# Kernel optimization log

Hardware: AMD Instinct MI355X
Metric: run time of the kernel (lower is better)

Reference implementation:

```python
import jax, jax.numpy as jnp
import numpy as np
from fractions import Fraction
from math import factorial

MUL = 64
IRREPS = [(MUL, 0, 1), (MUL, 1, -1), (MUL, 2, 1)]  # (mul, l, parity); same for in1/in2/out
N = 4096


def _f(n):
    return Fraction(factorial(round(n)), 1)


def _su2_cg(j1, m1, j2, m2, j3, m3):
    # Complex-basis SU(2) Clebsch-Gordan coefficient <j1 m1 j2 m2 | j3 m3> (Racah formula).
    if m3 != m1 + m2:
        return 0.0
    vmin = int(max(-j1 + j2 + m3, -j1 + m1, 0))
    vmax = int(min(j2 + j3 + m1, j3 - j1 + j2, j3 + m3))
    C = float((2 * j3 + 1) * Fraction(
        _f(j3 + j1 - j2) * _f(j3 - j1 + j2) * _f(j1 + j2 - j3) * _f(j3 + m3) * _f(j3 - m3),
        _f(j1 + j2 + j3 + 1) * _f(j1 - m1) * _f(j1 + m1) * _f(j2 - m2) * _f(j2 + m2))) ** 0.5
    S = Fraction(0)
    for v in range(vmin, vmax + 1):
        S += (-1) ** int(v + j2 + m2) * Fraction(
            _f(j2 + j3 + m1 - v) * _f(j1 - m1 + v),
            _f(v) * _f(j3 - j1 + j2 - v) * _f(j3 + m3 - v) * _f(v + j1 - j2 - m3))
    return C * float(S)


def _q(l):
    # Change of basis real -> complex spherical harmonics, with (-i)^l phase so CG is real.
    q = np.zeros((2 * l + 1, 2 * l + 1), dtype=complex)
    for m in range(-l, 0):
        q[l + m, l + abs(m)] = 1 / 2 ** 0.5
        q[l + m, l - abs(m)] = -1j / 2 ** 0.5
    q[l, l] = 1
    for m in range(1, l + 1):
        q[l + m, l + abs(m)] = (-1) ** m / 2 ** 0.5
        q[l + m, l - abs(m)] = 1j * (-1) ** m / 2 ** 0.5
    return (-1j) ** l * q


def _so3_cg(l1, l2, l3):
    # Real-basis SO(3) Clebsch-Gordan tensor, shape (2l1+1, 2l2+1, 2l3+1).
    C = np.zeros((2 * l1 + 1, 2 * l2 + 1, 2 * l3 + 1))
    for m1 in range(-l1, l1 + 1):
        for m2 in range(-l2, l2 + 1):
            for m3 in range(-l3, l3 + 1):
                C[l1 + m1, l2 + m2, l3 + m3] = _su2_cg(l1, m1, l2, m2, l3, m3)
    C = np.einsum('ij,kl,mn,ikm->jln', _q(l1), _q(l2), np.conj(_q(l3)), C)
    assert np.abs(C.imag).max() < 1e-6
    return np.ascontiguousarray(C.real.astype(np.float32))


def _offsets(irreps):
    offs, o = [], 0
    for mul, l, p in irreps:
        offs.append(o)
        o += mul * (2 * l + 1)
    return offs, o


OFF, DIM = _offsets(IRREPS)

# Enumerate fully-connected paths honoring parity and triangle selection rules.
PATHS = []
for io, (mo, lo, po) in enumerate(IRREPS):
    for i1, (m1, l1, p1) in enumerate(IRREPS):
        for i2, (m2, l2, p2) in enumerate(IRREPS):
            if p1 * p2 == po and abs(l1 - l2) <= lo <= l1 + l2:
                PATHS.append((i1, i2, io, _so3_cg(l1, l2, lo)))
N_PATHS = len(PATHS)  # 11 for this irrep layout


def setup_inputs() -> dict:
    key = jax.random.key(0)
    k1, k2, k3 = jax.random.split(key, 3)
    inputs1 = jax.random.normal(k1, (N, DIM), dtype=jnp.float32)
    inputs2 = jax.random.normal(k2, (N, DIM), dtype=jnp.float32)
    std = 1.0 / float(np.sqrt(MUL * MUL))  # per-path weight_std
    W = jax.random.normal(k3, (N_PATHS, MUL, MUL, MUL), dtype=jnp.float32) * std
    return {"inputs1": inputs1, "inputs2": inputs2, "W": W}


def _seg(x, i):
    mul, l, _ = IRREPS[i]
    d = 2 * l + 1
    return x[:, OFF[i]:OFF[i] + mul * d].reshape(x.shape[0], mul, d)


def reference(inputs1, inputs2, W):
    # out[z, w, k] = sum_{u,v,i,j} W_path[u,v,w] * CG[i,j,k] * x1[z,u,i] * x2[z,v,j]
    segs = [[] for _ in IRREPS]
    for p, (i1, i2, io, cg) in enumerate(PATHS):
        x1 = _seg(inputs1, i1)  # [z, u, i]
        x2 = _seg(inputs2, i2)  # [z, v, j]
        y = jnp.einsum('zui,zvj,ijk,uvw->zwk', x1, x2, jnp.asarray(cg), W[p], optimize=True)
        segs[io].append(y)
    out = jnp.concatenate(
        [sum(s).reshape(inputs1.shape[0], -1) for s in segs], axis=-1)
    # normalize=True: divide by sqrt(output dim), as in the source
    return out * (1.0 / float(np.sqrt(out.shape[-1])))
```

## Files before the change

kernel.cpp:

```cpp
#include <hip/hip_runtime.h>
#include <hip/hip_fp16.h>


typedef unsigned short u16;
typedef _Float16 f16;
typedef __attribute__((ext_vector_type(8))) _Float16 f16x8;
typedef __attribute__((ext_vector_type(4))) float f32x4;

#define NZ 4096
#define ROWE 832
#define ROW2 576

__device__ __forceinline__ u16 f2h(float x) {
    _Float16 v = (_Float16)x; u16 b; __builtin_memcpy(&b, &v, 2); return b;
}

constexpr u16 f2h_bits(float xf) {
    unsigned u = __builtin_bit_cast(unsigned, xf);
    unsigned sign = (u >> 16) & 0x8000u;
    int exp = (int)((u >> 23) & 0xffu) - 127 + 15;
    unsigned man = u & 0x7fffffu;
    if (exp >= 31) return (u16)(sign | 0x7c00u);
    if (exp <= 0) {
        if (exp < -10) return (u16)sign;
        man |= 0x800000u;
        int sh = 14 - exp;
        unsigned h = man >> sh;
        unsigned rem = man & ((1u << sh) - 1u);
        unsigned half = 1u << (sh - 1);
        if (rem > half || (rem == half && (h & 1u))) ++h;
        return (u16)(sign | h);
    }
    unsigned h = ((unsigned)exp << 10) | (man >> 13);
    unsigned rem = man & 0x1fffu;
    if (rem > 0x1000u || (rem == 0x1000u && (h & 1u))) ++h;
    return (u16)(sign | h);
}
__device__ __forceinline__ __half2 h2dup(unsigned bits16) {
    unsigned d = bits16 * 0x10001u;
    __half2 r; __builtin_memcpy(&r, &d, 4); return r;
}
__device__ __forceinline__ __half2 h2zero() {
    unsigned z = 0; __half2 r; __builtin_memcpy(&r, &z, 4); return r;
}

struct CGE { int i, j, k; float c; };
template<int P> struct CGT;
template<> struct CGT<0> { static constexpr int n=1; static constexpr CGE e[1]={{0,0,0,1.0f}}; };
template<> struct CGT<1> { static constexpr int n=3; static constexpr CGE e[3]={
    {0,0,0,0.5773502691896258f},{1,1,0,0.5773502691896258f},{2,2,0,0.5773502691896258f}}; };
template<> struct CGT<2> { static constexpr int n=5; static constexpr CGE e[5]={
    {0,0,0,0.4472135954999579f},{1,1,0,0.4472135954999579f},{2,2,0,0.4472135954999579f},
    {3,3,0,0.4472135954999579f},{4,4,0,0.4472135954999579f}}; };
template<> struct CGT<3> { static constexpr int n=3; static constexpr CGE e[3]={
    {0,0,0,1.0f},{0,1,1,1.0f},{0,2,2,1.0f}}; };
template<> struct CGT<4> { static constexpr int n=3; static constexpr CGE e[3]={
    {0,0,0,1.0f},{1,0,1,1.0f},{2,0,2,1.0f}}; };
template<> struct CGT<5> { static constexpr int n=11; static constexpr CGE e[11]={
    {0,2,0,-0.31622776601683794f},{1,1,0,0.5477225575051661f},{0,4,0,-0.5477225575051661f},{2,0,0,0.5477225575051661f},
    {0,1,1,0.5477225575051661f},{2,3,1,0.5477225575051661f},{1,2,1,0.6324555320336759f},
    {2,2,2,-0.31622776601683794f},{1,3,2,0.5477225575051661f},{0,0,2,0.5477225575051661f},{2,4,2,0.5477225575051661f}}; };
template<> struct CGT<6> { static constexpr int n=11; static constexpr CGE e[11]={
    {2,0,0,-0.31622776601683794f},{1,1,0,0.5477225575051661f},{4,0,0,-0.5477225575051661f},{0,2,0,0.5477225575051661f},
    {1,0,1,0.5477225575051661f},{3,2,1,0.5477225575051661f},{2,1,1,0.6324555320336759f},
    {2,2,2,-0.31622776601683794f},{3,1,2,0.5477225575051661f},{0,0,2,0.5477225575051661f},{4,2,2,0.5477225575051661f}}; };
template<> struct CGT<7> { static constexpr int n=5; static constexpr CGE e[5]={
    {0,0,0,1.0f},{0,1,1,1.0f},{0,2,2,1.0f},{0,3,3,1.0f},{0,4,4,1.0f}}; };
template<> struct CGT<8> { static constexpr int n=11; static constexpr CGE e[11]={
    {0,2,0,0.7071067811865476f},{2,0,0,0.7071067811865476f},
    {0,1,1,0.7071067811865476f},{1,0,1,0.7071067811865476f},
    {0,0,2,-0.4082482904638630f},{1,1,2,0.8164965809277260f},{2,2,2,-0.4082482904638630f},
    {1,2,3,0.7071067811865476f},{2,1,3,0.7071067811865476f},
    {0,0,4,-0.7071067811865476f},{2,2,4,0.7071067811865476f}}; };
template<> struct CGT<9> { static constexpr int n=5; static constexpr CGE e[5]={
    {0,0,0,1.0f},{1,0,1,1.0f},{2,0,2,1.0f},{3,0,3,1.0f},{4,0,4,1.0f}}; };
template<> struct CGT<10> { static constexpr int n=25; static constexpr CGE e[25]={
    {0,2,0,-0.5345224838248488f},{2,0,0,-0.5345224838248488f},{1,3,0,0.4629100498862757f},{3,1,0,0.4629100498862757f},
    {0,3,1,0.4629100498862757f},{3,0,1,0.4629100498862757f},{1,4,1,-0.4629100498862757f},{4,1,1,-0.4629100498862757f},
    {1,2,1,0.2672612419124244f},{2,1,1,0.2672612419124244f},
    {0,0,2,-0.5345224838248488f},{1,1,2,0.2672612419124244f},{2,2,2,0.5345224838248488f},{3,3,2,0.2672612419124244f},{4,4,2,-0.5345224838248488f},
    {0,1,3,0.4629100498862757f},{1,0,3,0.4629100498862757f},{3,4,3,0.4629100498862757f},{4,3,3,0.4629100498862757f},
    {2,3,3,0.2672612419124244f},{3,2,3,0.2672612419124244f},
    {1,1,4,-0.4629100498862757f},{3,3,4,0.4629100498862757f},{2,4,4,-0.5345224838248488f},{4,2,4,-0.5345224838248488f}}; };

template<int SEG>
__device__ __forceinline__ int soff(int m) {
    if constexpr (SEG == 0) return m;
    else if constexpr (SEG == 1) return 64 + 4*m;
    else return 320 + 8*m;
}
template<int SEG>
__device__ __forceinline__ int sb2(int j) {
    if constexpr (SEG == 0) return 0;
    else if constexpr (SEG == 1) return 64 + j*64;
    else return 256 + j*64;
}
template<int L>
__device__ __forceinline__ void load_a1bits(const u16* p, u16* o) {
    if constexpr (L == 0) {
        o[0] = p[0];
    } else if constexpr (L == 1) {
        uint2 r = *reinterpret_cast<const uint2*>(p);
        o[0] = (u16)(r.x & 0xffff); o[1] = (u16)(r.x >> 16); o[2] = (u16)(r.y & 0xffff);
    } else {
        uint4 r = *reinterpret_cast<const uint4*>(p);
        o[0] = (u16)(r.x & 0xffff); o[1] = (u16)(r.x >> 16);
        o[2] = (u16)(r.y & 0xffff); o[3] = (u16)(r.y >> 16);
        o[4] = (u16)(r.z & 0xffff);
    }
}

__device__ __forceinline__ void stage_chunk(const u16* __restrict__ Wtb, int g,
                                            u16* lbuf, int tid) {
    const u16* src = Wtb + ((size_t)g << 13);
    #pragma unroll
    for (int qq = 0; qq < 4; ++qq) {
        const int off = qq*2048 + tid*8;
        __builtin_amdgcn_global_load_lds(
            (const __attribute__((address_space(1))) void*)(const void*)(src + off),
            (__attribute__((address_space(3))) void*)(void*)(lbuf + off),
            16, 0, 0);
    }
}

template<int PID, int S1, int S2, int KO>
__device__ __forceinline__ void chunk_compute(const u16* __restrict__ lbuf,
                                              const u16 (&a1b)[2][2*S1+1],
                                              const __half2 (&b2h)[2][4][2*S2+1],
                                              f32x4 (&acc)[KO][4], int lane) {
    const int kb = lane >> 4, nl = lane & 15;
    #pragma unroll
    for (int uu = 0; uu < 2; ++uu) {
        __half2 a1h[2*S1+1];
        #pragma unroll
        for (int i = 0; i < 2*S1+1; ++i) a1h[i] = h2dup(a1b[uu][i]);
        __half2 pre[CGT<PID>::n];
        #pragma unroll
        for (int t = 0; t < CGT<PID>::n; ++t) {
            const u16 cb = f2h_bits(CGT<PID>::e[t].c);
            pre[t] = __hmul2(h2dup(cb), a1h[CGT<PID>::e[t].i]);
        }
        #pragma unroll
        for (int h = 0; h < 2; ++h) {
            f16x8 bf[4];
            #pragma unroll
            for (int nf = 0; nf < 4; ++nf) {
                const int w = nf*16 + nl;
                const int slot = w*16 + ((uu*8 + h*4 + kb) ^ (w & 15));
                bf[nf] = *reinterpret_cast<const f16x8*>(lbuf + slot*8);
            }
            #pragma unroll
            for (int ko = 0; ko < KO; ++ko) {
                union { __half2 h[4]; f16x8 v; } af;
                #pragma unroll
                for (int q = 0; q < 4; ++q) {
                    __half2 s = h2zero();
                    #pragma unroll
                    for (int t = 0; t < CGT<PID>::n; ++t)
                        if (CGT<PID>::e[t].k == ko)
                            s = __hfma2(pre[t], b2h[h][q][CGT<PID>::e[t].j], s);
                    af.h[q] = s;
                }
                #pragma unroll
                for (int nf = 0; nf < 4; ++nf)
                    acc[ko][nf] = __builtin_amdgcn_mfma_f32_16x16x32_f16(af.v, bf[nf], acc[ko][nf], 0, 0, 0);
            }
        }
    }
}

template<int PID, int S1, int S2, int KO>
__device__ __forceinline__ void run_path(const u16* __restrict__ x1r, const u16* __restrict__ x2r,
                                         const u16* __restrict__ Wtb, u16* lds,
                                         f32x4 (&acc)[KO][4], int lane, int tid,
                                         int cbase, int cpp, int& q, int nq, int GB) {
    constexpr int D1 = 2*S1 + 1, D2 = 2*S2 + 1;
    const int kb = lane >> 4;
    __half2 b2h[2][4][D2];
    #pragma unroll
    for (int h = 0; h < 2; ++h)
        #pragma unroll
        for (int j = 0; j < D2; ++j) {
            const u16* p = x2r + sb2<S2>(j) + h*32 + kb*8;
            uint4 r = *reinterpret_cast<const uint4*>(p);
            __builtin_memcpy(&b2h[h][0][j], &r.x, 4);
            __builtin_memcpy(&b2h[h][1][j], &r.y, 4);
            __builtin_memcpy(&b2h[h][2][j], &r.z, 4);
            __builtin_memcpy(&b2h[h][3][j], &r.w, 4);
        }

    const int ubase = cbase*2;
    u16 a1b[2][D1], a1nb[2][D1];
    #pragma unroll
    for (int uu = 0; uu < 2; ++uu)
        load_a1bits<S1>(x1r + soff<S1>(ubase + uu), a1b[uu]);

    for (int c = 0; c < cpp; ++c) {
        __syncthreads();
        const int cn = (c + 1 == cpp) ? 0 : c + 1;
        #pragma unroll
        for (int uu = 0; uu < 2; ++uu)
            load_a1bits<S1>(x1r + soff<S1>(ubase + cn*2 + uu), a1nb[uu]);
        if (q + 1 < nq) {
            const int qn = q + 1;
            const int g = GB + (qn/cpp)*32 + cbase + (qn % cpp);
            stage_chunk(Wtb, g, lds + ((qn & 1) << 13), tid);
        }
        chunk_compute<PID,S1,S2,KO>(lds + ((q & 1) << 13), a1b, b2h, acc, lane);
        #pragma unroll
        for (int uu = 0; uu < 2; ++uu)
            #pragma unroll
            for (int d = 0; d < D1; ++d) a1b[uu][d] = a1nb[uu][d];
        ++q;
    }
}

template<int IO, bool DIRECT>
__device__ __forceinline__ void run_unit(const u16* __restrict__ XB1, const u16* __restrict__ XB2,
                                         const u16* __restrict__ Wtb, float* __restrict__ dst,
                                         int zt, int cbase, int cpp, u16* lds) {
    constexpr int KO   = 2*IO + 1;
    constexpr int NP   = (IO == 0) ? 3 : 4;
    constexpr int GB   = (IO == 0) ? 0 : (IO == 1 ? 96 : 224);
    constexpr int OFFI = (IO == 0) ? 0 : (IO == 1 ? 64 : 256);
    constexpr int CO   = KO*64;
    const int tid = threadIdx.x;
    const int lane = tid & 63, wave = tid >> 6;
    const int zin = zt*64 + wave*16 + (lane & 15);
    const u16* x1r = XB1 + (size_t)zin*ROWE;
    const u16* x2r = XB2 + (size_t)zin*ROW2;
    f32x4 acc[KO][4];
    #pragma unroll
    for (int k = 0; k < KO; ++k)
        #pragma unroll
        for (int nf = 0; nf < 4; ++nf) acc[k][nf] = (f32x4){0.f, 0.f, 0.f, 0.f};

    int q = 0;
    const int nq = NP*cpp;
    stage_chunk(Wtb, GB + cbase, lds, tid);

    if constexpr (IO == 0) {
        run_path<0,0,0,KO>(x1r, x2r, Wtb, lds, acc, lane, tid, cbase, cpp, q, nq, GB);
        run_path<1,1,1,KO>(x1r, x2r, Wtb, lds, acc, lane, tid, cbase, cpp, q, nq, GB);
        run_path<2,2,2,KO>(x1r, x2r, Wtb, lds, acc, lane, tid, cbase, cpp, q, nq, GB);
    } else if constexpr (IO == 1) {
        run_path<3,0,1,KO>(x1r, x2r, Wtb, lds, acc, lane, tid, cbase, cpp, q, nq, GB);
        run_path<4,1,0,KO>(x1r, x2r, Wtb, lds, acc, lane, tid, cbase, cpp, q, nq, GB);
        run_path<5,1,2,KO>(x1r, x2r, Wtb, lds, acc, lane, tid, cbase, cpp, q, nq, GB);
        run_path<6,2,1,KO>(x1r, x2r, Wtb, lds, acc, lane, tid, cbase, cpp, q, nq, GB);
    } else {
        run_path<7,0,2,KO>(x1r, x2r, Wtb, lds, acc, lane, tid, cbase, cpp, q, nq, GB);
        run_path<8,1,1,KO>(x1r, x2r, Wtb, lds, acc, lane, tid, cbase, cpp, q, nq, GB);
        run_path<9,2,0,KO>(x1r, x2r, Wtb, lds, acc, lane, tid, cbase, cpp, q, nq, GB);
        run_path<10,2,2,KO>(x1r, x2r, Wtb, lds, acc, lane, tid, cbase, cpp, q, nq, GB);
    }

    float* lf = reinterpret_cast<float*>(lds);
    const int nl = lane & 15;
    const int hi = lane >> 4;
    #pragma unroll
    for (int round = 0; round < 4; ++round) {
        __syncthreads();
        if (wave == round) {
            const int zl = hi*4;
            #pragma unroll
            for (int k = 0; k < KO; ++k)
                #pragma unroll
                for (int nf = 0; nf < 4; ++nf) {
                    const int col = (nf*16 + nl)*KO + k;
                    #pragma unroll
                    for (int r = 0; r < 4; ++r)
                        lf[(zl + r)*CO + col] = acc[k][nf][r];
                }
        }
        __syncthreads();
        const int zbase = zt*64 + round*16;
        const int TOT4 = 4*CO;
        for (int i = tid; i < TOT4; i += 256) {
            const int zr = i / (CO/4), c4 = i % (CO/4);
            float4 v = *reinterpret_cast<const float4*>(&lf[zr*CO + c4*4]);
            if constexpr (DIRECT) {
                const float sc = 0.041666666666666664f;
                v.x *= sc; v.y *= sc; v.z *= sc; v.w *= sc;
            }
            *reinterpret_cast<float4*>(&dst[(size_t)(zbase + zr)*576 + OFFI + c4*4]) = v;
        }
    }
}

template<bool DEEP>
__global__ __launch_bounds__(256) void tp_main_split(const u16* __restrict__ XB1, const u16* __restrict__ XB2,
                                                     const u16* __restrict__ Wtb, float* __restrict__ Pbuf) {
    __shared__ u16 smem[2*8192];
    const int bid = blockIdx.x;
    int io, uq, zt, cbase, cpp;
    if constexpr (DEEP) {
        if (bid < 512)      { io = 2; uq = bid >> 6; zt = bid & 63; cbase = uq*4; cpp = 4; }
        else if (bid < 896) { const int b = bid - 512; io = 1; uq = b >> 6; zt = b & 63;
                              cbase = (uq < 2) ? uq*6 : 12 + (uq - 2)*5; cpp = (uq < 2) ? 6 : 5; }
        else                { const int b = bid - 896; io = 0; uq = b >> 6; zt = b & 63;
                              cbase = uq*8; cpp = 8; }
    } else {
        if (bid < 256)      { io = 2; uq = bid >> 6; zt = bid & 63; cbase = uq*8; cpp = 8; }
        else if (bid < 448) { const int b = bid - 256; io = 1; uq = b >> 6; zt = b & 63;
                              cbase = (uq == 0) ? 0 : (11 + 11*(uq - 1)); cpp = (uq == 2) ? 10 : 11; }
        else                { const int b = bid - 448; io = 0; uq = 0; zt = b & 63; cbase = 0; cpp = 32; }
    }
    float* dstP = Pbuf + (size_t)uq*NZ*576;
    if (io == 0)      run_unit<0,false>(XB1, XB2, Wtb, dstP, zt, cbase, cpp, smem);
    else if (io == 1) run_unit<1,false>(XB1, XB2, Wtb, dstP, zt, cbase, cpp, smem);
    else              run_unit<2,false>(XB1, XB2, Wtb, dstP, zt, cbase, cpp, smem);
}

__global__ __launch_bounds__(256) void tp_main_direct(const u16* __restrict__ XB1, const u16* __restrict__ XB2,
                                                      const u16* __restrict__ Wtb, float* __restrict__ out) {
    __shared__ u16 smem[2*8192];
    const int bid = blockIdx.x;
    const int io = 2 - (bid >> 6), zt = bid & 63;
    if (io == 0)      run_unit<0,true>(XB1, XB2, Wtb, out, zt, 0, 32, smem);
    else if (io == 1) run_unit<1,true>(XB1, XB2, Wtb, out, zt, 0, 32, smem);
    else              run_unit<2,true>(XB1, XB2, Wtb, out, zt, 0, 32, smem);
}

template<int CA, int CB, int CC>
__global__ __launch_bounds__(256) void reduce_k(const float* __restrict__ P, float* __restrict__ out) {
    const int i = blockIdx.x*256 + threadIdx.x;
    const int col0 = (i*4) % 576;
    const int cnt = (col0 < 64) ? CA : (col0 < 256 ? CB : CC);
    float4 s = reinterpret_cast<const float4*>(P)[i];
    for (int u = 1; u < cnt; ++u) {
        float4 t = reinterpret_cast<const float4*>(P + (size_t)u*NZ*576)[i];
        s.x += t.x; s.y += t.y; s.z += t.z; s.w += t.w;
    }
    const float sc = 0.041666666666666664f;
    float4 o; o.x = s.x*sc; o.y = s.y*sc; o.z = s.z*sc; o.w = s.w*sc;
    reinterpret_cast<float4*>(out)[i] = o;
}

__global__ void prep_x(const float* __restrict__ x1, const float* __restrict__ x2,
                       u16* __restrict__ XB1, u16* __restrict__ XB2) {
    int g = blockIdx.x * 256 + threadIdx.x;
    const int P1 = NZ * 192;
    const int P2 = NZ * 144;
    if (g < P1) {
        const int zz = g / 192, s = g - zz*192, seg = s >> 6, m = s & 63;
        const float* sp = x1 + (size_t)zz*576;
        u16* dp = XB1 + (size_t)zz*ROWE;
        if (seg == 0) {
            dp[m] = f2h(sp[m]);
        } else if (seg == 1) {
            u16 t0 = f2h(sp[64 + m*3 + 0]);
            u16 t1 = f2h(sp[64 + m*3 + 1]);
            u16 t2 = f2h(sp[64 + m*3 + 2]);
            uint2 pk; pk.x = (unsigned)t0 | ((unsigned)t1 << 16); pk.y = (unsigned)t2;
            *reinterpret_cast<uint2*>(dp + 64 + m*4) = pk;
        } else {
            u16 t[5];
            #pragma unroll
            for (int c = 0; c < 5; ++c) t[c] = f2h(sp[256 + m*5 + c]);
            uint4 pk;
            pk.x = (unsigned)t[0] | ((unsigned)t[1] << 16);
            pk.y = (unsigned)t[2] | ((unsigned)t[3] << 16);
            pk.z = (unsigned)t[4];
            pk.w = 0u;
            *reinterpret_cast<uint4*>(dp + 320 + m*8) = pk;
        }
    } else if (g < P1 + P2) {
        const int gg = g - P1;
        const int zz = gg / 144, c4 = gg - zz*144;
        const int col = c4*4;
        const float* sp = x2 + (size_t)zz*576;
        u16 t[4];
        #pragma unroll
        for (int qd = 0; qd < 4; ++qd) {
            const int cc = col + qd;
            int si;
            if (cc < 64)       si = cc;
            else if (cc < 256) { const int j = (cc - 64) >> 6, v = (cc - 64) & 63;  si = 64  + v*3 + j; }
            else               { const int j = (cc - 256) >> 6, v = (cc - 256) & 63; si = 256 + v*5 + j; }
            t[qd] = f2h(sp[si]);
        }
        uint2 pk;
        pk.x = (unsigned)t[0] | ((unsigned)t[1] << 16);
        pk.y = (unsigned)t[2] | ((unsigned)t[3] << 16);
        *reinterpret_cast<uint2*>(XB2 + (size_t)zz*ROW2 + col) = pk;
    }
}

__global__ void prep_w(const float* __restrict__ W, u16* __restrict__ Wtb) {
    __shared__ float ld[4096];
    const int b = blockIdx.x;
    const int p = b >> 6, u = b & 63;
    const int tid = threadIdx.x;
    const float* src = W + ((size_t)(p*64 + u) << 12);
    #pragma unroll
    for (int i = 0; i < 16; ++i) ld[tid + i*256] = src[tid + i*256];
    __syncthreads();
    const int g  = p*32 + (u >> 1);
    const int mb = (u & 1)*8;
    #pragma unroll
    for (int r = 0; r < 2; ++r) {
        const int j = r*256 + tid;
        const int w = j & 63, ms = j >> 6;
        const int m = mb + ms;
        const int h = ms >> 2, kb = ms & 3;
        const int vb = h*32 + kb*8;
        u16 tmp[8];
        #pragma unroll
        for (int e = 0; e < 8; ++e) tmp[e] = f2h(ld[(vb + e)*64 + w]);
        const int unit = w*16 + (m ^ (w & 15));
        uint4 pk;
        pk.x = (unsigned)tmp[0] | ((unsigned)tmp[1] << 16);
        pk.y = (unsigned)tmp[2] | ((unsigned)tmp[3] << 16);
        pk.z = (unsigned)tmp[4] | ((unsigned)tmp[5] << 16);
        pk.w = (unsigned)tmp[6] | ((unsigned)tmp[7] << 16);
        *reinterpret_cast<uint4*>(Wtb + (size_t)g*8192 + (size_t)unit*8) = pk;
    }
}

extern "C" void kernel_launch(void* const* d_in, const int* in_sizes, int n_in,
                              void* d_out, int out_size, void* d_ws, size_t ws_size,
                              hipStream_t stream) {
    const float* x1 = (const float*)d_in[0];
    const float* x2 = (const float*)d_in[1];
    const float* W  = (const float*)d_in[2];
    float* out = (float*)d_out;

    u16* XB1 = (u16*)d_ws;
    u16* XB2 = XB1 + (size_t)NZ*ROWE;
    u16* Wtb = XB2 + (size_t)NZ*ROW2;
    const size_t baseu = (size_t)NZ*ROWE + (size_t)NZ*ROW2 + (size_t)11*32*8192;
    if (ws_size < baseu*2) return;
    float* Pbuf = (float*)(XB1 + baseu);
    const size_t avail = ws_size - baseu*2;
    const size_t psz = (size_t)NZ*576*4;
    const bool deep     = (avail >= 8*psz);
    const bool balanced = (avail >= 4*psz);

    hipLaunchKernelGGL(prep_x, dim3((NZ*(192+144))/256), dim3(256), 0, stream, x1, x2, XB1, XB2);
    hipLaunchKernelGGL(prep_w, dim3(11*64), dim3(256), 0, stream, W, Wtb);

    if (deep) {
        hipLaunchKernelGGL(tp_main_split<true>, dim3(1152), dim3(256), 0, stream, XB1, XB2, Wtb, Pbuf);
        hipLaunchKernelGGL((reduce_k<4,6,8>), dim3(NZ*576/4/256), dim3(256), 0, stream, Pbuf, out);
    } else if (balanced) {
        hipLaunchKernelGGL(tp_main_split<false>, dim3(512), dim3(256), 0, stream, XB1, XB2, Wtb, Pbuf);
        hipLaunchKernelGGL((reduce_k<1,3,4>), dim3(NZ*576/4/256), dim3(256), 0, stream, Pbuf, out);
    } else {
        hipLaunchKernelGGL(tp_main_direct, dim3(192), dim3(256), 0, stream, XB1, XB2, Wtb, out);
    }
}
```

Baseline: 118.6 us.

## Halve weight chunk granularity and rebalance split-K work across fewer blocks

Each staged weight chunk now covers one u row (4096 halves) instead of two, with the prep_w layout, swizzle, chunk indexing and LDS buffers reworked to match, which shrinks the shared-memory footprint. The deep 1152-block split is removed. The balanced path now launches 576 blocks with 2/3/4 partial slices per output irrep, so the reduction reads fewer partials. The aim is higher occupancy from less LDS and less partial-sum traffic. The cost is twice as many barriers and chunk stages per unit of work, plus fewer blocks to hide latency.

```diff
diff --git a/kernel.cpp b/kernel.cpp
--- a/kernel.cpp
+++ b/kernel.cpp
@@ -112,9 +112,9 @@
 
 __device__ __forceinline__ void stage_chunk(const u16* __restrict__ Wtb, int g,
                                             u16* lbuf, int tid) {
-    const u16* src = Wtb + ((size_t)g << 13);
-    #pragma unroll
-    for (int qq = 0; qq < 4; ++qq) {
+    const u16* src = Wtb + ((size_t)g << 12);
+    #pragma unroll
+    for (int qq = 0; qq < 2; ++qq) {
         const int off = qq*2048 + tid*8;
         __builtin_amdgcn_global_load_lds(
             (const __attribute__((address_space(1))) void*)(const void*)(src + off),
@@ -125,46 +125,43 @@
 
 template<int PID, int S1, int S2, int KO>
 __device__ __forceinline__ void chunk_compute(const u16* __restrict__ lbuf,
-                                              const u16 (&a1b)[2][2*S1+1],
+                                              const u16 (&a1b)[2*S1+1],
                                               const __half2 (&b2h)[2][4][2*S2+1],
                                               f32x4 (&acc)[KO][4], int lane) {
     const int kb = lane >> 4, nl = lane & 15;
-    #pragma unroll
-    for (int uu = 0; uu < 2; ++uu) {
-        __half2 a1h[2*S1+1];
-        #pragma unroll
-        for (int i = 0; i < 2*S1+1; ++i) a1h[i] = h2dup(a1b[uu][i]);
-        __half2 pre[CGT<PID>::n];
-        #pragma unroll
-        for (int t = 0; t < CGT<PID>::n; ++t) {
-            const u16 cb = f2h_bits(CGT<PID>::e[t].c);
-            pre[t] = __hmul2(h2dup(cb), a1h[CGT<PID>::e[t].i]);
-        }
-        #pragma unroll
-        for (int h = 0; h < 2; ++h) {
-            f16x8 bf[4];
+    __half2 a1h[2*S1+1];
+    #pragma unroll
+    for (int i = 0; i < 2*S1+1; ++i) a1h[i] = h2dup(a1b[i]);
+    __half2 pre[CGT<PID>::n];
+    #pragma unroll
+    for (int t = 0; t < CGT<PID>::n; ++t) {
+        const u16 cb = f2h_bits(CGT<PID>::e[t].c);
+        pre[t] = __hmul2(h2dup(cb), a1h[CGT<PID>::e[t].i]);
+    }
+    #pragma unroll
+    for (int h = 0; h < 2; ++h) {
+        f16x8 bf[4];
+        #pragma unroll
+        for (int nf = 0; nf < 4; ++nf) {
+            const int w = nf*16 + nl;
+            const int slot = w*8 + ((h*4 + kb) ^ (w & 7));
+            bf[nf] = *reinterpret_cast<const f16x8*>(lbuf + slot*8);
+        }
+        #pragma unroll
+        for (int ko = 0; ko < KO; ++ko) {
+            union { __half2 h[4]; f16x8 v; } af;
             #pragma unroll
-            for (int nf = 0; nf < 4; ++nf) {
-                const int w = nf*16 + nl;
-                const int slot = w*16 + ((uu*8 + h*4 + kb) ^ (w & 15));
-                bf[nf] = *reinterpret_cast<const f16x8*>(lbuf + slot*8);
+            for (int q = 0; q < 4; ++q) {
+                __half2 s = h2zero();
+                #pragma unroll
+                for (int t = 0; t < CGT<PID>::n; ++t)
+                    if (CGT<PID>::e[t].k == ko)
+                        s = __hfma2(pre[t], b2h[h][q][CGT<PID>::e[t].j], s);
+                af.h[q] = s;
             }
             #pragma unroll
-            for (int ko = 0; ko < KO; ++ko) {
-                union { __half2 h[4]; f16x8 v; } af;
-                #pragma unroll
-                for (int q = 0; q < 4; ++q) {
-                    __half2 s = h2zero();
-                    #pragma unroll
-                    for (int t = 0; t < CGT<PID>::n; ++t)
-                        if (CGT<PID>::e[t].k == ko)
-                            s = __hfma2(pre[t], b2h[h][q][CGT<PID>::e[t].j], s);
-                    af.h[q] = s;
-                }
-                #pragma unroll
-                for (int nf = 0; nf < 4; ++nf)
-                    acc[ko][nf] = __builtin_amdgcn_mfma_f32_16x16x32_f16(af.v, bf[nf], acc[ko][nf], 0, 0, 0);
-            }
+            for (int nf = 0; nf < 4; ++nf)
+                acc[ko][nf] = __builtin_amdgcn_mfma_f32_16x16x32_f16(af.v, bf[nf], acc[ko][nf], 0, 0, 0);
         }
     }
 }
@@ -189,28 +186,21 @@
             __builtin_memcpy(&b2h[h][3][j], &r.w, 4);
         }
 
-    const int ubase = cbase*2;
-    u16 a1b[2][D1], a1nb[2][D1];
-    #pragma unroll
-    for (int uu = 0; uu < 2; ++uu)
-        load_a1bits<S1>(x1r + soff<S1>(ubase + uu), a1b[uu]);
+    u16 a1b[D1], a1nb[D1];
+    load_a1bits<S1>(x1r + soff<S1>(cbase), a1b);
 
     for (int c = 0; c < cpp; ++c) {
         __syncthreads();
         const int cn = (c + 1 == cpp) ? 0 : c + 1;
-        #pragma unroll
-        for (int uu = 0; uu < 2; ++uu)
-            load_a1bits<S1>(x1r + soff<S1>(ubase + cn*2 + uu), a1nb[uu]);
+        load_a1bits<S1>(x1r + soff<S1>(cbase + cn), a1nb);
         if (q + 1 < nq) {
             const int qn = q + 1;
-            const int g = GB + (qn/cpp)*32 + cbase + (qn % cpp);
-            stage_chunk(Wtb, g, lds + ((qn & 1) << 13), tid);
-        }
-        chunk_compute<PID,S1,S2,KO>(lds + ((q & 1) << 13), a1b, b2h, acc, lane);
-        #pragma unroll
-        for (int uu = 0; uu < 2; ++uu)
-            #pragma unroll
-            for (int d = 0; d < D1; ++d) a1b[uu][d] = a1nb[uu][d];
+            const int g = GB + (qn/cpp)*64 + cbase + (qn % cpp);
+            stage_chunk(Wtb, g, lds + ((qn & 1) << 12), tid);
+        }
+        chunk_compute<PID,S1,S2,KO>(lds + ((q & 1) << 12), a1b, b2h, acc, lane);
+        #pragma unroll
+        for (int d = 0; d < D1; ++d) a1b[d] = a1nb[d];
         ++q;
     }
 }
@@ -221,7 +211,7 @@
                                          int zt, int cbase, int cpp, u16* lds) {
     constexpr int KO   = 2*IO + 1;
     constexpr int NP   = (IO == 0) ? 3 : 4;
-    constexpr int GB   = (IO == 0) ? 0 : (IO == 1 ? 96 : 224);
+    constexpr int GB   = (IO == 0) ? 0 : (IO == 1 ? 192 : 448);
     constexpr int OFFI = (IO == 0) ? 0 : (IO == 1 ? 64 : 256);
     constexpr int CO   = KO*64;
     const int tid = threadIdx.x;
@@ -288,24 +278,16 @@
     }
 }
 
-template<bool DEEP>
 __global__ __launch_bounds__(256) void tp_main_split(const u16* __restrict__ XB1, const u16* __restrict__ XB2,
                                                      const u16* __restrict__ Wtb, float* __restrict__ Pbuf) {
-    __shared__ u16 smem[2*8192];
+    __shared__ u16 smem[12288];
     const int bid = blockIdx.x;
     int io, uq, zt, cbase, cpp;
-    if constexpr (DEEP) {
-        if (bid < 512)      { io = 2; uq = bid >> 6; zt = bid & 63; cbase = uq*4; cpp = 4; }
-        else if (bid < 896) { const int b = bid - 512; io = 1; uq = b >> 6; zt = b & 63;
-                              cbase = (uq < 2) ? uq*6 : 12 + (uq - 2)*5; cpp = (uq < 2) ? 6 : 5; }
-        else                { const int b = bid - 896; io = 0; uq = b >> 6; zt = b & 63;
-                              cbase = uq*8; cpp = 8; }
-    } else {
-        if (bid < 256)      { io = 2; uq = bid >> 6; zt = bid & 63; cbase = uq*8; cpp = 8; }
-        else if (bid < 448) { const int b = bid - 256; io = 1; uq = b >> 6; zt = b & 63;
-                              cbase = (uq == 0) ? 0 : (11 + 11*(uq - 1)); cpp = (uq == 2) ? 10 : 11; }
-        else                { const int b = bid - 448; io = 0; uq = 0; zt = b & 63; cbase = 0; cpp = 32; }
-    }
+    if (bid < 256)      { io = 2; uq = bid >> 6; zt = bid & 63; cbase = uq*16; cpp = 16; }
+    else if (bid < 448) { const int b = bid - 256; io = 1; uq = b >> 6; zt = b & 63;
+                          cbase = (uq == 0) ? 0 : (22 + 21*(uq - 1)); cpp = (uq == 0) ? 22 : 21; }
+    else                { const int b = bid - 448; io = 0; uq = b >> 6; zt = b & 63;
+                          cbase = uq*32; cpp = 32; }
     float* dstP = Pbuf + (size_t)uq*NZ*576;
     if (io == 0)      run_unit<0,false>(XB1, XB2, Wtb, dstP, zt, cbase, cpp, smem);
     else if (io == 1) run_unit<1,false>(XB1, XB2, Wtb, dstP, zt, cbase, cpp, smem);
@@ -314,12 +296,12 @@
 
 __global__ __launch_bounds__(256) void tp_main_direct(const u16* __restrict__ XB1, const u16* __restrict__ XB2,
                                                       const u16* __restrict__ Wtb, float* __restrict__ out) {
-    __shared__ u16 smem[2*8192];
+    __shared__ u16 smem[12288];
     const int bid = blockIdx.x;
     const int io = 2 - (bid >> 6), zt = bid & 63;
-    if (io == 0)      run_unit<0,true>(XB1, XB2, Wtb, out, zt, 0, 32, smem);
-    else if (io == 1) run_unit<1,true>(XB1, XB2, Wtb, out, zt, 0, 32, smem);
-    else              run_unit<2,true>(XB1, XB2, Wtb, out, zt, 0, 32, smem);
+    if (io == 0)      run_unit<0,true>(XB1, XB2, Wtb, out, zt, 0, 64, smem);
+    else if (io == 1) run_unit<1,true>(XB1, XB2, Wtb, out, zt, 0, 64, smem);
+    else              run_unit<2,true>(XB1, XB2, Wtb, out, zt, 0, 64, smem);
 }
 
 template<int CA, int CB, int CC>
@@ -396,25 +378,23 @@
     #pragma unroll
     for (int i = 0; i < 16; ++i) ld[tid + i*256] = src[tid + i*256];
     __syncthreads();
-    const int g  = p*32 + (u >> 1);
-    const int mb = (u & 1)*8;
+    const int g = p*64 + u;
     #pragma unroll
     for (int r = 0; r < 2; ++r) {
         const int j = r*256 + tid;
         const int w = j & 63, ms = j >> 6;
-        const int m = mb + ms;
         const int h = ms >> 2, kb = ms & 3;
         const int vb = h*32 + kb*8;
         u16 tmp[8];
         #pragma unroll
         for (int e = 0; e < 8; ++e) tmp[e] = f2h(ld[(vb + e)*64 + w]);
-        const int unit = w*16 + (m ^ (w & 15));
+        const int unit = w*8 + (ms ^ (w & 7));
         uint4 pk;
         pk.x = (unsigned)tmp[0] | ((unsigned)tmp[1] << 16);
         pk.y = (unsigned)tmp[2] | ((unsigned)tmp[3] << 16);
         pk.z = (unsigned)tmp[4] | ((unsigned)tmp[5] << 16);
         pk.w = (unsigned)tmp[6] | ((unsigned)tmp[7] << 16);
-        *reinterpret_cast<uint4*>(Wtb + (size_t)g*8192 + (size_t)unit*8) = pk;
+        *reinterpret_cast<uint4*>(Wtb + (size_t)g*4096 + (size_t)unit*8) = pk;
     }
 }
 
@@ -429,23 +409,19 @@
     u16* XB1 = (u16*)d_ws;
     u16* XB2 = XB1 + (size_t)NZ*ROWE;
     u16* Wtb = XB2 + (size_t)NZ*ROW2;
-    const size_t baseu = (size_t)NZ*ROWE + (size_t)NZ*ROW2 + (size_t)11*32*8192;
+    const size_t baseu = (size_t)NZ*ROWE + (size_t)NZ*ROW2 + (size_t)11*64*4096;
     if (ws_size < baseu*2) return;
     float* Pbuf = (float*)(XB1 + baseu);
     const size_t avail = ws_size - baseu*2;
     const size_t psz = (size_t)NZ*576*4;
-    const bool deep     = (avail >= 8*psz);
     const bool balanced = (avail >= 4*psz);
 
     hipLaunchKernelGGL(prep_x, dim3((NZ*(192+144))/256), dim3(256), 0, stream, x1, x2, XB1, XB2);
     hipLaunchKernelGGL(prep_w, dim3(11*64), dim3(256), 0, stream, W, Wtb);
 
-    if (deep) {
-        hipLaunchKernelGGL(tp_main_split<true>, dim3(1152), dim3(256), 0, stream, XB1, XB2, Wtb, Pbuf);
-        hipLaunchKernelGGL((reduce_k<4,6,8>), dim3(NZ*576/4/256), dim3(256), 0, stream, Pbuf, out);
-    } else if (balanced) {
-        hipLaunchKernelGGL(tp_main_split<false>, dim3(512), dim3(256), 0, stream, XB1, XB2, Wtb, Pbuf);
-        hipLaunchKernelGGL((reduce_k<1,3,4>), dim3(NZ*576/4/256), dim3(256), 0, stream, Pbuf, out);
+    if (balanced) {
+        hipLaunchKernelGGL(tp_main_split, dim3(576), dim3(256), 0, stream, XB1, XB2, Wtb, Pbuf);
+        hipLaunchKernelGGL((reduce_k<2,3,4>), dim3(NZ*576/4/256), dim3(256), 0, stream, Pbuf, out);
     } else {
         hipLaunchKernelGGL(tp_main_direct, dim3(192), dim3(256), 0, stream, XB1, XB2, Wtb, out);
     }
```

After: 130.6 us. 1.1x slower.
